# Kernel optimization log

Measured on AMD Instinct MI355X. Metric: run time of the kernel, lower is better.

## Reference

```python
import jax, jax.numpy as jnp
import numpy as np

B, C1, C2, HEADS = 8, 256, 512, 8
HD = C1 // HEADS
H3, W3, H4, W4 = 128, 128, 64, 64
EPS = 1e-5

def _ln(x, g, b):
    m = jnp.mean(x, -1, keepdims=True)
    v = jnp.mean((x - m) ** 2, -1, keepdims=True)
    return (x - m) * jax.lax.rsqrt(v + EPS) * g + b

def _pool(x, k):
    b, c, h, w = x.shape
    return x.reshape(b, c, h // k, k, w // k, k).mean(axis=(3, 5))

def _resize(x, h, w):
    b, c = x.shape[:2]
    return jax.image.resize(x, (b, c, h, w), method='bilinear')

def setup_inputs():
    key = jax.random.key(0)
    ks = jax.random.split(key, 12)
    w = lambda k, s: jax.random.normal(k, s, jnp.float32) * 0.02
    z = lambda *s: jnp.zeros(s, jnp.float32)
    o = lambda *s: jnp.ones(s, jnp.float32)
    return {
        'a3': jax.random.normal(ks[0], (B, C1, H3, W3), jnp.float32),
        'a4': jax.random.normal(ks[1], (B, C2, H4, W4), jnp.float32),
        'conv_w': w(ks[2], (C1, C2)), 'conv_b': z(C1),
        'bn_g': o(C1), 'bn_b': z(C1), 'bn_rm': z(C1), 'bn_rv': o(C1),
        'wq': w(ks[3], (C1, C1)), 'bq': z(C1), 'lnq_g': o(C1), 'lnq_b': z(C1),
        'wk': w(ks[4], (C1, C1)), 'bk': z(C1), 'lnk_g': o(C1), 'lnk_b': z(C1),
        'wv': w(ks[5], (C1, C1)), 'bv': z(C1),
        'wo': w(ks[6], (C1, C1)), 'bo': z(C1),
        'w1': w(ks[7], (4 * C1, C1)), 'b1': z(4 * C1),
        'w2': w(ks[8], (C1, 4 * C1)), 'b2': z(C1),
        'n1_g': o(C1), 'n1_b': z(C1), 'n2_g': o(C1), 'n2_b': z(C1),
        'idx': 11,
    }

def _forward(a3, a4, conv_w, conv_b, bn_g, bn_b, bn_rm, bn_rv, wq, bq, lnq_g, lnq_b,
             wk, bk, lnk_g, lnk_b, wv, bv, wo, bo, w1, b1, w2, b2,
             n1_g, n1_b, n2_g, n2_b, idx):
    # 1x1 conv (high_to_low_embed) + eval-mode BatchNorm2d
    a4e = jnp.einsum('bchw,oc->bohw', a4, conv_w) + conv_b[:, None, None]
    a4e = (a4e - bn_rm[:, None, None]) * (bn_g * jax.lax.rsqrt(bn_rv + EPS))[:, None, None] + bn_b[:, None, None]
    if idx == 11:
        a3d = _pool(a3, 2)
    else:
        a3d = _pool(a3, 4)
        a4e = _pool(a4e, 2)
    b, c, h, w = a3d.shape
    H, W = a4e.shape[2:]
    a3f = a3d.reshape(b, c, h * w).transpose(0, 2, 1)   # [b, Nq, c1]
    a4f = a4e.reshape(b, c, H * W).transpose(0, 2, 1)   # [b, Nk, c1]
    Q = _ln(a3f @ wq.T + bq, lnq_g, lnq_b)
    K = _ln(a4f @ wk.T + bk, lnk_g, lnk_b)
    V = a4f @ wv.T + bv
    Q = jax.nn.relu(Q.reshape(b, h * w, HEADS, HD).transpose(0, 2, 3, 1))  # [b,h,d,Nq]
    K = jax.nn.relu(K.reshape(b, H * W, HEADS, HD).transpose(0, 2, 3, 1))  # [b,h,d,Nk]
    V = V.reshape(b, H * W, HEADS, HD).transpose(0, 2, 3, 1)               # [b,h,d,Nk]
    V = jnp.pad(V, ((0, 0), (0, 0), (0, 1), (0, 0)), constant_values=1.0)  # [b,h,d+1,Nk]
    VK = jnp.einsum('bhen,bhdn->bhed', V, K)            # [b,h,d+1,d]
    out = jnp.einsum('bhed,bhdq->bheq', VK, Q)          # [b,h,d+1,Nq]
    denom = jnp.maximum(out[:, :, -1:], EPS)            # clamp(min=eps)
    out = out[:, :, :-1] / denom                        # [b,h,d,Nq]
    # replicate torch: out.transpose(1,2).contiguous().view(bs,-1,heads*head_dim)
    out = jnp.swapaxes(out, 1, 2).reshape(b, h * w, HEADS * HD)
    out = out @ wo.T + bo
    # transformer FFN branch: computed by the original module but not in its returned outputs
    src = _ln(a3f + out, n1_g, n1_b)
    ffn = jax.nn.gelu(src @ w1.T + b1, approximate=False) @ w2.T + b2
    src = _ln(src + ffn, n2_g, n2_b)
    del src  # dead in original return as well
    a3_sa = out.transpose(0, 2, 1).reshape(b, c, h, w)
    a3_sa = _resize(a3_sa, a3.shape[2], a3.shape[3]) * a3
    a4_up = _resize(a4, a4.shape[2] * 2, a4.shape[3] * 2)
    return a3_sa, a4_up

def reference(a3, a4, conv_w, conv_b, bn_g, bn_b, bn_rm, bn_rv, wq, bq, lnq_g, lnq_b,
              wk, bk, lnk_g, lnk_b, wv, bv, wo, bo, w1, b1, w2, b2,
              n1_g, n1_b, n2_g, n2_b, idx):
    return _forward(a3, a4, conv_w, conv_b, bn_g, bn_b, bn_rm, bn_rv, wq, bq, lnq_g, lnq_b,
                    wk, bk, lnk_g, lnk_b, wv, bv, wo, bo, w1, b1, w2, b2,
                    n1_g, n1_b, n2_g, n2_b, idx)
```

## Files before the change

### kernel.cpp

```cpp
#include <hip/hip_runtime.h>
#include <cstdint>
#include <cstddef>

typedef unsigned short u16;
typedef __bf16 bf16x8 __attribute__((ext_vector_type(8)));
typedef float f32x4 __attribute__((ext_vector_type(4)));

#define EPS_ 1e-5f

__device__ __forceinline__ float bf2f(u16 u){
  union { uint32_t i; float f; } v; v.i = ((uint32_t)u) << 16; return v.f;
}
__device__ __forceinline__ u16 f2bf(float f){
  union { float f; uint32_t i; } v; v.f = f;
  uint32_t u = v.i;
  u += 0x7fffu + ((u >> 16) & 1u);
  return (u16)(u >> 16);
}
__device__ __forceinline__ void gload_lds16(const void* g, void* l){
  __builtin_amdgcn_global_load_lds((const __attribute__((address_space(1))) uint32_t*)g,
                                   (__attribute__((address_space(3))) uint32_t*)l, 16, 0, 0);
}

#define OFF_WKV   ((size_t)0)
#define OFF_WQB   ((size_t)524288)
#define OFF_WOB   ((size_t)655360)
#define OFF_BKV   ((size_t)786432)
#define OFF_A3DT  ((size_t)2097152)
#define OFF_Q     ((size_t)18874368)

#define OUT1_A4T  ((size_t)0)
#define OUT1_KV   ((size_t)33554432)
#define OUT1_ATT  ((size_t)67108864)
#define OUT1_PROJ ((size_t)83886080)
#define OUT1_VK   ((size_t)117440512)
#define OUT1_VKB  ((size_t)121765888)

__global__ __launch_bounds__(256) void k_fold(
    const float* __restrict__ conv_w, const float* __restrict__ conv_b,
    const float* __restrict__ bn_g, const float* __restrict__ bn_b,
    const float* __restrict__ bn_rm, const float* __restrict__ bn_rv,
    const float* __restrict__ wk, const float* __restrict__ bk,
    const float* __restrict__ wv, const float* __restrict__ bv,
    u16* __restrict__ WKV, float* __restrict__ bkv){
  int n = blockIdx.x;
  int t = threadIdx.x;
  const float* wrow = (n < 256) ? (wk + (size_t)n*256) : (wv + (size_t)(n-256)*256);
  __shared__ float sw[256], st_[256];
  {
    float s  = bn_g[t] * rsqrtf(bn_rv[t] + EPS_);
    float tt = s * (conv_b[t] - bn_rm[t]) + bn_b[t];
    float w = wrow[t];
    sw[t] = w * s;
    st_[t] = w * tt;
  }
  __syncthreads();
  for (int cc = 0; cc < 2; ++cc){
    int c = t + cc*256;
    float acc = 0.f;
    #pragma unroll 8
    for (int o = 0; o < 256; ++o)
      acc += sw[o] * conv_w[(size_t)o*512 + c];
    WKV[(size_t)n*512 + c] = f2bf(acc);
  }
  if (t == 0){
    float acc = (n < 256) ? bk[n] : bv[n-256];
    for (int o = 0; o < 256; ++o) acc += st_[o];
    bkv[n] = acc;
  }
}

__global__ __launch_bounds__(256) void k_cvt(const float* __restrict__ src, u16* __restrict__ dst){
  int i = blockIdx.x*256 + threadIdx.x;
  dst[i] = f2bf(src[i]);
}

__global__ __launch_bounds__(256) void k_pool_a3(const float* __restrict__ a3, u16* __restrict__ a3dT){
  int y = blockIdx.x;
  int c0 = blockIdx.y * 32;
  int b = blockIdx.z;
  int t = threadIdx.x;
  __shared__ float ld[32*257];
  const float* src = a3 + (((size_t)(b*256 + c0))*128 + 2*y)*128;
  #pragma unroll
  for (int cc = 0; cc < 32; ++cc)
    ld[cc*257 + t] = src[(size_t)cc*16384 + t];
  __syncthreads();
  int cc = t & 31, xb = t >> 5;
  u16* dst = a3dT + ((size_t)b*4096 + y*64)*256 + c0 + cc;
  #pragma unroll
  for (int xi = 0; xi < 8; ++xi){
    int x = xb*8 + xi;
    const float* r = &ld[cc*257 + 2*x];
    float v = 0.25f*(r[0] + r[1] + r[128] + r[129]);
    dst[(size_t)x*256] = f2bf(v);
  }
}

__global__ __launch_bounds__(256) void k_tr_a4(const float* __restrict__ a4, u16* __restrict__ a4T){
  int y = blockIdx.x;
  int c0 = blockIdx.y * 32;
  int b = blockIdx.z;
  int t = threadIdx.x;
  __shared__ float ld[32*65];
  const float* src = a4 + (((size_t)(b*512 + c0))*64 + y)*64;
  #pragma unroll
  for (int i = 0; i < 8; ++i){
    int idx = i*256 + t;
    int cc = idx >> 6, x = idx & 63;
    ld[cc*65 + x] = src[(size_t)cc*4096 + x];
  }
  __syncthreads();
  int cc = t & 31, xb = t >> 5;
  u16* dst = a4T + ((size_t)b*4096 + y*64)*512 + c0 + cc;
  #pragma unroll
  for (int xi = 0; xi < 8; ++xi){
    int x = xb*8 + xi;
    dst[(size_t)x*512] = f2bf(ld[cc*65 + x]);
  }
}

template<int KDIM, int NDIM, int SMODE>
__global__ __launch_bounds__(256) void k_gemm(
    const u16* __restrict__ A, const u16* __restrict__ Bw,
    const float* __restrict__ bias, void* __restrict__ Cout){
  __shared__ alignas(16) u16 lA[128*32];
  __shared__ alignas(16) u16 lB[128*32];
  int m0 = blockIdx.x * 128, n0 = blockIdx.y * 128;
  int t = threadIdx.x;
  int lane = t & 63, wid = t >> 6;
  int wm = wid >> 1, wn = wid & 1;
  int fr = lane & 15, fq = lane >> 4;
  f32x4 acc[4][4] = {};
  const u16* Abase = A + (size_t)m0 * KDIM;
  const u16* Bbase = Bw + (size_t)n0 * KDIM;
  for (int kt = 0; kt < KDIM/32; ++kt){
    #pragma unroll
    for (int i = 0; i < 2; ++i){
      int u = i*256 + t;
      gload_lds16(Abase + (size_t)(u>>2)*KDIM + kt*32 + (u&3)*8, lA + u*8);
      gload_lds16(Bbase + (size_t)(u>>2)*KDIM + kt*32 + (u&3)*8, lB + u*8);
    }
    __syncthreads();
    bf16x8 af[4], bfr[4];
    #pragma unroll
    for (int fm = 0; fm < 4; ++fm)
      af[fm] = *(const bf16x8*)&lA[(wm*64 + fm*16 + fr)*32 + fq*8];
    #pragma unroll
    for (int fn = 0; fn < 4; ++fn)
      bfr[fn] = *(const bf16x8*)&lB[(wn*64 + fn*16 + fr)*32 + fq*8];
    #pragma unroll
    for (int fm = 0; fm < 4; ++fm)
      #pragma unroll
      for (int fn = 0; fn < 4; ++fn)
        acc[fm][fn] = __builtin_amdgcn_mfma_f32_16x16x32_bf16(af[fm], bfr[fn], acc[fm][fn], 0, 0, 0);
    __syncthreads();
  }
  #pragma unroll
  for (int fn = 0; fn < 4; ++fn){
    int j = n0 + wn*64 + fn*16 + fr;
    float bj = bias[j];
    #pragma unroll
    for (int fm = 0; fm < 4; ++fm){
      int m = m0 + wm*64 + fm*16 + fq*4;
      if constexpr (SMODE == 0){
        u16* C = (u16*)Cout;
        #pragma unroll
        for (int i = 0; i < 4; ++i)
          C[(size_t)(m + i)*NDIM + j] = f2bf(acc[fm][fn][i] + bj);
      } else {
        int b = m >> 12, p = m & 4095;
        size_t base = ((size_t)(b*NDIM + j))*4096 + p;
        if constexpr (SMODE == 1){
          u16* C = (u16*)Cout;
          ushort4 pk;
          pk.x = f2bf(acc[fm][fn][0] + bj);
          pk.y = f2bf(acc[fm][fn][1] + bj);
          pk.z = f2bf(acc[fm][fn][2] + bj);
          pk.w = f2bf(acc[fm][fn][3] + bj);
          *(ushort4*)&C[base] = pk;
        } else {
          float* C = (float*)Cout;
          float4 o4;
          o4.x = acc[fm][fn][0] + bj; o4.y = acc[fm][fn][1] + bj;
          o4.z = acc[fm][fn][2] + bj; o4.w = acc[fm][fn][3] + bj;
          *(float4*)&C[base] = o4;
        }
      }
    }
  }
}

__global__ __launch_bounds__(256) void k_ln_row(u16* __restrict__ X,
    const float* __restrict__ g, const float* __restrict__ bb){
  int row = blockIdx.x*4 + (threadIdx.x >> 6);
  int lane = threadIdx.x & 63;
  u16* p = X + (size_t)row*256 + lane*4;
  ushort4 v4 = *(const ushort4*)p;
  float v0 = bf2f(v4.x), v1 = bf2f(v4.y), v2 = bf2f(v4.z), v3 = bf2f(v4.w);
  float s = v0+v1+v2+v3;
  float s2 = v0*v0+v1*v1+v2*v2+v3*v3;
  #pragma unroll
  for (int off = 32; off > 0; off >>= 1){
    s  += __shfl_down(s, off);
    s2 += __shfl_down(s2, off);
  }
  s = __shfl(s, 0); s2 = __shfl(s2, 0);
  float mean = s * (1.f/256.f);
  float var = s2 * (1.f/256.f) - mean*mean;
  float r = rsqrtf(var + EPS_);
  float4 gg = *(const float4*)&g[lane*4];
  float4 b4 = *(const float4*)&bb[lane*4];
  ushort4 o;
  o.x = f2bf(fmaxf((v0-mean)*r*gg.x + b4.x, 0.f));
  o.y = f2bf(fmaxf((v1-mean)*r*gg.y + b4.y, 0.f));
  o.z = f2bf(fmaxf((v2-mean)*r*gg.z + b4.z, 0.f));
  o.w = f2bf(fmaxf((v3-mean)*r*gg.w + b4.w, 0.f));
  *(ushort4*)p = o;
}

__global__ __launch_bounds__(256) void k_ln_col(u16* __restrict__ KV,
    const float* __restrict__ g, const float* __restrict__ bb){
  int p0 = blockIdx.x * 128;
  int b = blockIdx.y;
  int t = threadIdx.x;
  int pl = t & 127, jh = t >> 7;
  u16* base = KV + (size_t)b*512*4096 + p0 + pl;
  float s = 0.f, s2 = 0.f;
  for (int jj = 0; jj < 128; ++jj){
    float v = bf2f(base[(size_t)(jh*128 + jj)*4096]);
    s += v; s2 += v*v;
  }
  __shared__ float sh[2][2][128];
  sh[0][jh][pl] = s; sh[1][jh][pl] = s2;
  __syncthreads();
  float st = sh[0][0][pl] + sh[0][1][pl];
  float s2t = sh[1][0][pl] + sh[1][1][pl];
  float mean = st * (1.f/256.f);
  float var = s2t * (1.f/256.f) - mean*mean;
  float r = rsqrtf(var + EPS_);
  for (int jj = 0; jj < 128; ++jj){
    int j = jh*128 + jj;
    u16* q = base + (size_t)j*4096;
    float v = bf2f(*q);
    *q = f2bf(fmaxf((v - mean)*r*g[j] + bb[j], 0.f));
  }
}

__global__ __launch_bounds__(64) void k_vk(const u16* __restrict__ KV, float* __restrict__ VKp){
  int chunk = blockIdx.x;
  int bh = blockIdx.y;
  int b = bh >> 3, h = bh & 7;
  int lane = threadIdx.x;
  __shared__ alignas(16) u16 lK[32*256];
  __shared__ alignas(16) u16 lV[32*256];
  int n0 = chunk * 256;
  const u16* Ks = KV + ((size_t)(b*512 + h*32))*4096 + n0;
  const u16* Vs = KV + ((size_t)(b*512 + 256 + h*32))*4096 + n0;
  #pragma unroll
  for (int i = 0; i < 16; ++i){
    int u = i*64 + lane;
    int row = u >> 5, cb = (u & 31)*8;
    gload_lds16(Ks + (size_t)row*4096 + cb, lK + u*8);
    gload_lds16(Vs + (size_t)row*4096 + cb, lV + u*8);
  }
  __builtin_amdgcn_s_waitcnt(0);
  __syncthreads();
  int fr = lane & 15, fq = lane >> 4;
  f32x4 acc[2][2] = {};
  #pragma unroll
  for (int ks = 0; ks < 8; ++ks){
    bf16x8 av0 = *(const bf16x8*)&lV[(fr)*256 + ks*32 + fq*8];
    bf16x8 av1 = *(const bf16x8*)&lV[(16+fr)*256 + ks*32 + fq*8];
    bf16x8 bk0 = *(const bf16x8*)&lK[(fr)*256 + ks*32 + fq*8];
    bf16x8 bk1 = *(const bf16x8*)&lK[(16+fr)*256 + ks*32 + fq*8];
    acc[0][0] = __builtin_amdgcn_mfma_f32_16x16x32_bf16(av0, bk0, acc[0][0], 0,0,0);
    acc[0][1] = __builtin_amdgcn_mfma_f32_16x16x32_bf16(av0, bk1, acc[0][1], 0,0,0);
    acc[1][0] = __builtin_amdgcn_mfma_f32_16x16x32_bf16(av1, bk0, acc[1][0], 0,0,0);
    acc[1][1] = __builtin_amdgcn_mfma_f32_16x16x32_bf16(av1, bk1, acc[1][1], 0,0,0);
  }
  float* dst = VKp + ((size_t)bh*16 + chunk)*(33*32);
  #pragma unroll
  for (int fe = 0; fe < 2; ++fe)
    #pragma unroll
    for (int fd = 0; fd < 2; ++fd)
      #pragma unroll
      for (int i = 0; i < 4; ++i){
        int e = fe*16 + fq*4 + i;
        int d = fd*16 + fr;
        dst[e*32 + d] = acc[fe][fd][i];
      }
  {
    int d = lane & 31, half = lane >> 5;
    float s = 0.f;
    #pragma unroll
    for (int i = 0; i < 16; ++i){
      bf16x8 kv = *(const bf16x8*)&lK[d*256 + half*128 + i*8];
      #pragma unroll
      for (int j = 0; j < 8; ++j) s += (float)kv[j];
    }
    s += __shfl_down(s, 32);
    if (lane < 32) dst[32*32 + d] = s;
  }
}

__global__ __launch_bounds__(256) void k_cvt_vk(const float* __restrict__ VKp, u16* __restrict__ VKb){
  int i = blockIdx.x*256 + threadIdx.x;
  int bh = i / (48*32);
  int r = i - bh*48*32;
  int e = r >> 5, d = r & 31;
  float v = 0.f;
  if (e < 33){
    const float* p = VKp + (size_t)bh*16*(33*32) + e*32 + d;
    #pragma unroll
    for (int c = 0; c < 16; ++c) v += p[(size_t)c*(33*32)];
  }
  VKb[i] = f2bf(v);
}

__global__ __launch_bounds__(256) void k_att(const u16* __restrict__ Q,
    const u16* __restrict__ VKb, u16* __restrict__ ATT){
  int qc = blockIdx.x;
  int bh = blockIdx.y;
  int b = bh >> 3, h = bh & 7;
  int t = threadIdx.x;
  int lane = t & 63, wid = t >> 6;
  int fr = lane & 15, fq = lane >> 4;
  int q0 = qc*256 + wid*64;
  const u16* Qb = Q + ((size_t)(b*4096 + q0))*256 + h*32 + fq*8;
  bf16x8 aq[4];
  #pragma unroll
  for (int fm = 0; fm < 4; ++fm)
    aq[fm] = *(const bf16x8*)&Qb[(size_t)(fm*16 + fr)*256];
  const u16* Vb = VKb + (size_t)bh*48*32;
  bf16x8 bv_[3];
  #pragma unroll
  for (int fn = 0; fn < 3; ++fn)
    bv_[fn] = *(const bf16x8*)&Vb[(fn*16 + fr)*32 + fq*8];
  f32x4 acc[4][3] = {};
  #pragma unroll
  for (int fm = 0; fm < 4; ++fm)
    #pragma unroll
    for (int fn = 0; fn < 3; ++fn)
      acc[fm][fn] = __builtin_amdgcn_mfma_f32_16x16x32_bf16(aq[fm], bv_[fn], acc[fm][fn], 0,0,0);
  __shared__ alignas(16) u16 latt[32*264];
  #pragma unroll
  for (int fm = 0; fm < 4; ++fm){
    #pragma unroll
    for (int i = 0; i < 4; ++i){
      float dv = __shfl(acc[fm][2][i], lane & 48);
      float rd = 1.0f / fmaxf(dv, EPS_);
      int qloc = wid*64 + fm*16 + fq*4 + i;
      latt[(fr)*264 + qloc]      = f2bf(acc[fm][0][i] * rd);
      latt[(16 + fr)*264 + qloc] = f2bf(acc[fm][1][i] * rd);
    }
  }
  __syncthreads();
  int row = t >> 3, seg = t & 7;
  u16* dst = ATT + ((size_t)(b*4096 + row*128 + h*16 + qc))*256 + seg*32;
  const u16* srcl = &latt[row*264 + seg*32];
  #pragma unroll
  for (int k = 0; k < 4; ++k)
    *(uint4*)&dst[k*8] = *(const uint4*)&srcl[k*8];
}

__device__ __forceinline__ void bil_idx(int o, int n, int &i0, int &i1, float &w0, float &w1){
  float s = 0.5f*(float)o - 0.25f;
  float fl = floorf(s);
  i0 = (int)fl; i1 = i0 + 1;
  w1 = s - fl; w0 = 1.f - w1;
  if (i0 < 0){ i0 = 0; w0 = 0.f; w1 = 1.f; }
  if (i1 > n-1){ i1 = n-1; w1 = 0.f; w0 = 1.f; }
}

__global__ __launch_bounds__(256) void k_resize_mul_a3(const float* __restrict__ PROJ,
    const float* __restrict__ a3, float* __restrict__ out0){
  int bc = blockIdx.x;
  int t = threadIdx.x;
  __shared__ float P[4096];
  const float* src = PROJ + (size_t)bc*4096;
  #pragma unroll
  for (int i = 0; i < 16; ++i) P[i*256 + t] = src[i*256 + t];
  __syncthreads();
  const float* ap = a3 + (size_t)bc*16384;
  float* op = out0 + (size_t)bc*16384;
  for (int k = 0; k < 64; ++k){
    int px = k*256 + t;
    int Y = px >> 7, X = px & 127;
    int y0,y1,x0,x1; float wy0,wy1,wx0,wx1;
    bil_idx(Y, 64, y0,y1,wy0,wy1);
    bil_idx(X, 64, x0,x1,wx0,wx1);
    float v = wy0*(wx0*P[y0*64+x0] + wx1*P[y0*64+x1])
            + wy1*(wx0*P[y1*64+x0] + wx1*P[y1*64+x1]);
    op[px] = v * ap[px];
  }
}

__global__ __launch_bounds__(256) void k_resize_a4(const float* __restrict__ a4, float* __restrict__ out1){
  int bc = blockIdx.x;
  int t = threadIdx.x;
  __shared__ float P[4096];
  const float* src = a4 + (size_t)bc*4096;
  #pragma unroll
  for (int i = 0; i < 16; ++i) P[i*256 + t] = src[i*256 + t];
  __syncthreads();
  float* op = out1 + (size_t)bc*16384;
  for (int k = 0; k < 64; ++k){
    int px = k*256 + t;
    int Y = px >> 7, X = px & 127;
    int y0,y1,x0,x1; float wy0,wy1,wx0,wx1;
    bil_idx(Y, 64, y0,y1,wy0,wy1);
    bil_idx(X, 64, x0,x1,wx0,wx1);
    op[px] = wy0*(wx0*P[y0*64+x0] + wx1*P[y0*64+x1])
           + wy1*(wx0*P[y1*64+x0] + wx1*P[y1*64+x1]);
  }
}

extern "C" void kernel_launch(void* const* d_in, const int* in_sizes, int n_in,
                              void* d_out, int out_size, void* d_ws, size_t ws_size,
                              hipStream_t stream){
  (void)in_sizes; (void)n_in; (void)out_size; (void)ws_size;
  const float* a3     = (const float*)d_in[0];
  const float* a4     = (const float*)d_in[1];
  const float* conv_w = (const float*)d_in[2];
  const float* conv_b = (const float*)d_in[3];
  const float* bn_g   = (const float*)d_in[4];
  const float* bn_b   = (const float*)d_in[5];
  const float* bn_rm  = (const float*)d_in[6];
  const float* bn_rv  = (const float*)d_in[7];
  const float* wq     = (const float*)d_in[8];
  const float* bq     = (const float*)d_in[9];
  const float* lnq_g  = (const float*)d_in[10];
  const float* lnq_b  = (const float*)d_in[11];
  const float* wk     = (const float*)d_in[12];
  const float* bk     = (const float*)d_in[13];
  const float* lnk_g  = (const float*)d_in[14];
  const float* lnk_b  = (const float*)d_in[15];
  const float* wv     = (const float*)d_in[16];
  const float* bv     = (const float*)d_in[17];
  const float* wo     = (const float*)d_in[18];
  const float* bo     = (const float*)d_in[19];

  float* out0 = (float*)d_out;
  float* out1 = out0 + (size_t)33554432;

  char* ws = (char*)d_ws;
  u16*   WKV  = (u16*)(ws + OFF_WKV);
  u16*   WQB  = (u16*)(ws + OFF_WQB);
  u16*   WOB  = (u16*)(ws + OFF_WOB);
  float* BKV  = (float*)(ws + OFF_BKV);
  u16*   A3DT = (u16*)(ws + OFF_A3DT);
  u16*   Qw   = (u16*)(ws + OFF_Q);

  char* o1 = (char*)out1;
  u16*   A4T  = (u16*)(o1 + OUT1_A4T);
  u16*   KVw  = (u16*)(o1 + OUT1_KV);
  u16*   ATT  = (u16*)(o1 + OUT1_ATT);
  float* PROJ = (float*)(o1 + OUT1_PROJ);
  float* VKp  = (float*)(o1 + OUT1_VK);
  u16*   VKB  = (u16*)(o1 + OUT1_VKB);

  k_fold<<<512, 256, 0, stream>>>(conv_w, conv_b, bn_g, bn_b, bn_rm, bn_rv,
                                  wk, bk, wv, bv, WKV, BKV);
  k_cvt<<<256, 256, 0, stream>>>(wq, WQB);
  k_cvt<<<256, 256, 0, stream>>>(wo, WOB);

  k_pool_a3<<<dim3(64, 8, 8), 256, 0, stream>>>(a3, A3DT);
  k_tr_a4<<<dim3(64, 16, 8), 256, 0, stream>>>(a4, A4T);

  k_gemm<256, 256, 0><<<dim3(256, 2), 256, 0, stream>>>(A3DT, WQB, bq, (void*)Qw);
  k_gemm<512, 512, 1><<<dim3(256, 4), 256, 0, stream>>>(A4T, WKV, BKV, (void*)KVw);

  k_ln_row<<<8192, 256, 0, stream>>>(Qw, lnq_g, lnq_b);
  k_ln_col<<<dim3(32, 8), 256, 0, stream>>>(KVw, lnk_g, lnk_b);

  k_vk<<<dim3(16, 64), 64, 0, stream>>>(KVw, VKp);
  k_cvt_vk<<<384, 256, 0, stream>>>(VKp, VKB);
  k_att<<<dim3(16, 64), 256, 0, stream>>>(Qw, VKB, ATT);

  k_gemm<256, 256, 2><<<dim3(256, 2), 256, 0, stream>>>(ATT, WOB, bo, (void*)PROJ);

  k_resize_mul_a3<<<2048, 256, 0, stream>>>(PROJ, a3, out0);
  k_resize_a4<<<4096, 256, 0, stream>>>(a4, out1);
}
```

Measured before the change: 801.0 us.

## Tile column LayerNorm through LDS, store projection as bf16, merge weight casts

```diff
diff --git a/kernel.cpp b/kernel.cpp
--- a/kernel.cpp
+++ b/kernel.cpp
@@ -70,8 +70,12 @@
   }
 }
 
-__global__ __launch_bounds__(256) void k_cvt(const float* __restrict__ src, u16* __restrict__ dst){
-  int i = blockIdx.x*256 + threadIdx.x;
+__global__ __launch_bounds__(256) void k_cvt2(const float* __restrict__ wq, const float* __restrict__ wo,
+                                              u16* __restrict__ WQB, u16* __restrict__ WOB){
+  int bidx = blockIdx.x;
+  const float* src = (bidx < 256) ? wq : wo;
+  u16* dst = (bidx < 256) ? WQB : WOB;
+  int i = (bidx & 255)*256 + threadIdx.x;
   dst[i] = f2bf(src[i]);
 }
 
@@ -171,21 +175,13 @@
       } else {
         int b = m >> 12, p = m & 4095;
         size_t base = ((size_t)(b*NDIM + j))*4096 + p;
-        if constexpr (SMODE == 1){
-          u16* C = (u16*)Cout;
-          ushort4 pk;
-          pk.x = f2bf(acc[fm][fn][0] + bj);
-          pk.y = f2bf(acc[fm][fn][1] + bj);
-          pk.z = f2bf(acc[fm][fn][2] + bj);
-          pk.w = f2bf(acc[fm][fn][3] + bj);
-          *(ushort4*)&C[base] = pk;
-        } else {
-          float* C = (float*)Cout;
-          float4 o4;
-          o4.x = acc[fm][fn][0] + bj; o4.y = acc[fm][fn][1] + bj;
-          o4.z = acc[fm][fn][2] + bj; o4.w = acc[fm][fn][3] + bj;
-          *(float4*)&C[base] = o4;
-        }
+        u16* C = (u16*)Cout;
+        ushort4 pk;
+        pk.x = f2bf(acc[fm][fn][0] + bj);
+        pk.y = f2bf(acc[fm][fn][1] + bj);
+        pk.z = f2bf(acc[fm][fn][2] + bj);
+        pk.w = f2bf(acc[fm][fn][3] + bj);
+        *(ushort4*)&C[base] = pk;
       }
     }
   }
@@ -224,26 +220,51 @@
   int p0 = blockIdx.x * 128;
   int b = blockIdx.y;
   int t = threadIdx.x;
-  int pl = t & 127, jh = t >> 7;
-  u16* base = KV + (size_t)b*512*4096 + p0 + pl;
-  float s = 0.f, s2 = 0.f;
-  for (int jj = 0; jj < 128; ++jj){
-    float v = bf2f(base[(size_t)(jh*128 + jj)*4096]);
-    s += v; s2 += v*v;
-  }
-  __shared__ float sh[2][2][128];
-  sh[0][jh][pl] = s; sh[1][jh][pl] = s2;
-  __syncthreads();
-  float st = sh[0][0][pl] + sh[0][1][pl];
-  float s2t = sh[1][0][pl] + sh[1][1][pl];
-  float mean = st * (1.f/256.f);
-  float var = s2t * (1.f/256.f) - mean*mean;
-  float r = rsqrtf(var + EPS_);
-  for (int jj = 0; jj < 128; ++jj){
-    int j = jh*128 + jj;
-    u16* q = base + (size_t)j*4096;
-    float v = bf2f(*q);
-    *q = f2bf(fmaxf((v - mean)*r*g[j] + bb[j], 0.f));
+  __shared__ uint32_t lds32[256*66];
+  __shared__ float sA[256], sB[256];
+  __shared__ float meanA[128], rstdA[128];
+  u16* tile = (u16*)lds32;
+  int c = t & 63;
+  int w = t >> 6;
+  #pragma unroll 8
+  for (int i = 0; i < 64; ++i){
+    int j = i*4 + w;
+    uint32_t v = ((const uint32_t*)(KV + ((size_t)(b*512 + j))*4096 + p0))[c];
+    lds32[j*66 + c] = v;
+  }
+  __syncthreads();
+  {
+    int p = t & 127, jh = t >> 7;
+    float s = 0.f, s2 = 0.f;
+    #pragma unroll 8
+    for (int jj = 0; jj < 128; ++jj){
+      float v = bf2f(tile[(jh*128 + jj)*132 + p]);
+      s += v; s2 += v*v;
+    }
+    sA[t] = s; sB[t] = s2;
+  }
+  __syncthreads();
+  if (t < 128){
+    float st = sA[t] + sA[128 + t];
+    float s2t = sB[t] + sB[128 + t];
+    float mean = st * (1.f/256.f);
+    float var = s2t * (1.f/256.f) - mean*mean;
+    meanA[t] = mean;
+    rstdA[t] = rsqrtf(var + EPS_);
+  }
+  __syncthreads();
+  float m0v = meanA[2*c], m1v = meanA[2*c + 1];
+  float r0 = rstdA[2*c], r1 = rstdA[2*c + 1];
+  #pragma unroll 8
+  for (int i = 0; i < 64; ++i){
+    int j = i*4 + w;
+    uint32_t v = lds32[j*66 + c];
+    float v0 = bf2f((u16)(v & 0xffffu));
+    float v1 = bf2f((u16)(v >> 16));
+    float gj = g[j], bj = bb[j];
+    u16 o0 = f2bf(fmaxf((v0 - m0v)*r0*gj + bj, 0.f));
+    u16 o1 = f2bf(fmaxf((v1 - m1v)*r1*gj + bj, 0.f));
+    ((uint32_t*)(KV + ((size_t)(b*512 + j))*4096 + p0))[c] = (uint32_t)o0 | ((uint32_t)o1 << 16);
   }
 }
 
@@ -373,14 +394,18 @@
   if (i1 > n-1){ i1 = n-1; w1 = 0.f; w0 = 1.f; }
 }
 
-__global__ __launch_bounds__(256) void k_resize_mul_a3(const float* __restrict__ PROJ,
+__global__ __launch_bounds__(256) void k_resize_mul_a3(const u16* __restrict__ PROJ,
     const float* __restrict__ a3, float* __restrict__ out0){
   int bc = blockIdx.x;
   int t = threadIdx.x;
   __shared__ float P[4096];
-  const float* src = PROJ + (size_t)bc*4096;
-  #pragma unroll
-  for (int i = 0; i < 16; ++i) P[i*256 + t] = src[i*256 + t];
+  const uint32_t* src = (const uint32_t*)(PROJ + (size_t)bc*4096);
+  #pragma unroll
+  for (int i = 0; i < 8; ++i){
+    uint32_t v = src[i*256 + t];
+    P[(i*256 + t)*2]     = bf2f((u16)(v & 0xffffu));
+    P[(i*256 + t)*2 + 1] = bf2f((u16)(v >> 16));
+  }
   __syncthreads();
   const float* ap = a3 + (size_t)bc*16384;
   float* op = out0 + (size_t)bc*16384;
@@ -456,14 +481,13 @@
   u16*   A4T  = (u16*)(o1 + OUT1_A4T);
   u16*   KVw  = (u16*)(o1 + OUT1_KV);
   u16*   ATT  = (u16*)(o1 + OUT1_ATT);
-  float* PROJ = (float*)(o1 + OUT1_PROJ);
+  u16*   PROJ = (u16*)(o1 + OUT1_PROJ);
   float* VKp  = (float*)(o1 + OUT1_VK);
   u16*   VKB  = (u16*)(o1 + OUT1_VKB);
 
   k_fold<<<512, 256, 0, stream>>>(conv_w, conv_b, bn_g, bn_b, bn_rm, bn_rv,
                                   wk, bk, wv, bv, WKV, BKV);
-  k_cvt<<<256, 256, 0, stream>>>(wq, WQB);
-  k_cvt<<<256, 256, 0, stream>>>(wo, WOB);
+  k_cvt2<<<512, 256, 0, stream>>>(wq, wo, WQB, WOB);
 
   k_pool_a3<<<dim3(64, 8, 8), 256, 0, stream>>>(a3, A3DT);
   k_tr_a4<<<dim3(64, 16, 8), 256, 0, stream>>>(a4, A4T);
@@ -478,7 +502,7 @@
   k_cvt_vk<<<384, 256, 0, stream>>>(VKp, VKB);
   k_att<<<dim3(16, 64), 256, 0, stream>>>(Qw, VKB, ATT);
 
-  k_gemm<256, 256, 2><<<dim3(256, 2), 256, 0, stream>>>(ATT, WOB, bo, (void*)PROJ);
+  k_gemm<256, 256, 1><<<dim3(256, 2), 256, 0, stream>>>(ATT, WOB, bo, (void*)PROJ);
 
   k_resize_mul_a3<<<2048, 256, 0, stream>>>(PROJ, a3, out0);
   k_resize_a4<<<4096, 256, 0, stream>>>(a4, out1);
```

Result: no change. 785.5 us (-1.9%).
